# Kernel tuning notes

Measured on AMD Instinct MI355X. Metric: run time of the kernel, lower is better.

Reference implementation:

```python
import jax, jax.numpy as jnp
import numpy as np

TEMP = 0.5   # temperature from __init__
EPS = 1e-8   # torch.nn.CosineSimilarity eps


def setup_inputs() -> dict:
    key = jax.random.key(0)
    N, D = 8192, 256
    x = jax.random.normal(key, (N, D), dtype=jnp.float32)
    # pairs: each label appears exactly twice, as required for the
    # sim[~mask].reshape(N, -1) in the original to be well-formed
    y = jnp.arange(N, dtype=jnp.int32) // 2
    return {"x": x, "y": y}


def reference(x, y):
    # cosine similarity matrix: normalize once, then one NxD @ DxN matmul
    # (equivalent to CosineSimilarity(x.unsqueeze(1), x.unsqueeze(0)) without
    #  the NxNxD intermediate)
    norm = jnp.maximum(jnp.linalg.norm(x, axis=1, keepdims=True), EPS)
    xn = x / norm
    sim = (xn @ xn.T) / TEMP                     # [N, N]

    # Original: positives = equal-label entries (row-major order, includes the
    # diagonal), logits = [positives | negatives] which is just a per-row
    # permutation of sim; labels = 0 -> CE target is the FIRST equal-label
    # column of each row. logsumexp is over the full row (all N entries).
    eq = y[:, None] == y[None, :]                # [N, N] bool
    first_pos = jnp.argmax(eq, axis=1)           # first column j with y_j == y_i
    target = jnp.take_along_axis(sim, first_pos[:, None], axis=1)[:, 0]  # [N]

    lse = jax.nn.logsumexp(sim, axis=1)          # [N]
    N = x.shape[0]
    loss = jnp.sum(lse - target) / N             # CrossEntropyLoss(sum) / N
    return loss
```

## Files before the change

kernel.cpp:

```cpp
#include <hip/hip_runtime.h>
#include <hip/hip_bf16.h>

#define D 256
#define INV_TEMP 2.0f

typedef __attribute__((ext_vector_type(8))) short short8;
typedef __attribute__((ext_vector_type(4))) float floatx4;

__device__ __forceinline__ unsigned short f2bf(float f) {
    union { float f; unsigned u; } a; a.f = f;
    unsigned r = (a.u + 0x7fffu + ((a.u >> 16) & 1u)) >> 16;
    return (unsigned short)r;
}

__device__ __forceinline__ void gload_lds16(const unsigned short* g,
                                            unsigned short* l) {
    __builtin_amdgcn_global_load_lds(
        (const __attribute__((address_space(1))) unsigned int*)g,
        (__attribute__((address_space(3))) unsigned int*)l, 16, 0, 0);
}

__global__ void nt_prep_kernel(const float* __restrict__ x,
                               unsigned short* __restrict__ xnb,
                               float* __restrict__ pair_dot) {
    int p    = blockIdx.x * 4 + (threadIdx.x >> 6);
    int lane = threadIdx.x & 63;
    const float4* a4 = (const float4*)(x + (size_t)(2 * p) * D);
    const float4* b4 = (const float4*)(x + (size_t)(2 * p + 1) * D);
    float4 a = a4[lane], b = b4[lane];
    float saa = a.x * a.x + a.y * a.y + a.z * a.z + a.w * a.w;
    float sbb = b.x * b.x + b.y * b.y + b.z * b.z + b.w * b.w;
    float sab = a.x * b.x + a.y * b.y + a.z * b.z + a.w * b.w;
    #pragma unroll
    for (int off = 32; off; off >>= 1) {
        saa += __shfl_xor(saa, off);
        sbb += __shfl_xor(sbb, off);
        sab += __shfl_xor(sab, off);
    }
    float inva = 1.0f / fmaxf(sqrtf(saa), 1e-8f);
    float invb = 1.0f / fmaxf(sqrtf(sbb), 1e-8f);
    ushort4 oa, ob;
    oa.x = f2bf(a.x * inva); oa.y = f2bf(a.y * inva);
    oa.z = f2bf(a.z * inva); oa.w = f2bf(a.w * inva);
    ob.x = f2bf(b.x * invb); ob.y = f2bf(b.y * invb);
    ob.z = f2bf(b.z * invb); ob.w = f2bf(b.w * invb);
    ((ushort4*)(xnb + (size_t)(2 * p) * D))[lane] = oa;
    ((ushort4*)(xnb + (size_t)(2 * p + 1) * D))[lane] = ob;
    if (lane == 0)
        pair_dot[p] = sab * inva * invb * INV_TEMP;
}

__global__ __launch_bounds__(256, 2)
void nt_simexp_kernel(const unsigned short* __restrict__ xnb,
                      float* __restrict__ contrib) {
    __shared__ __align__(16) unsigned short Bs[128 * 256];
    __shared__ __align__(16) unsigned short As[2][128 * 32];

    const int p  = blockIdx.x >> 4, q = blockIdx.x & 15;
    const int s1 = 63 - p;
    const int c0 = 64 - p;
    const int q0 = (p + q) & 15;

    const int tid  = threadIdx.x;
    const int wave = tid >> 6, lane = tid & 63;
    const int wm   = wave & 1, wn = wave >> 1;
    const int quad = lane >> 4, c = lane & 15;

    auto strip_of = [&](int i) { return (i < c0) ? p : s1; };
    auto bi_of    = [&](int i) { return (i < c0) ? (p + i) : (s1 + i - c0); };

    auto load_B = [&](int bj) {
        const unsigned short* src = xnb + (size_t)(bj * 128) * D;
        int rs = lane >> 5, pp = lane & 31;
        #pragma unroll
        for (int t = 0; t < 16; ++t) {
            int wl = wave * 16 + t;
            int rr = wl * 2 + rs;
            int j  = (pp & ~7) | ((pp ^ rr) & 7);
            gload_lds16(src + (size_t)rr * D + j * 8, Bs + wl * 512 + lane * 8);
        }
    };
    auto load_A = [&](int bi, int ph, unsigned short* Ab) {
        const unsigned short* src = xnb + (size_t)(bi * 128) * D + ph * 32;
        int rl = lane >> 2, pq = lane & 3;
        #pragma unroll
        for (int t = 0; t < 2; ++t) {
            int wl = wave * 2 + t;
            int rr = wl * 16 + rl;
            int j  = pq ^ ((rr >> 1) & 3);
            gload_lds16(src + (size_t)rr * D + j * 8, Ab + wl * 512 + lane * 8);
        }
    };

    floatx4 acc[4][4];
    auto compute = [&](const unsigned short* Ab, int ph) {
        const int pA = quad ^ ((c >> 1) & 3);
        const int jg = ph * 4 + quad;
        const int pB = (jg & ~7) | ((jg ^ c) & 7);
        short8 af[4], bf[4];
        #pragma unroll
        for (int mt = 0; mt < 4; ++mt)
            af[mt] = *(const short8*)(Ab + (wm * 64 + mt * 16 + c) * 32 + pA * 8);
        #pragma unroll
        for (int nt = 0; nt < 4; ++nt)
            bf[nt] = *(const short8*)(Bs + (wn * 64 + nt * 16 + c) * 256 + pB * 8);
        #pragma unroll
        for (int mt = 0; mt < 4; ++mt)
            #pragma unroll
            for (int nt = 0; nt < 4; ++nt)
                acc[mt][nt] = __builtin_amdgcn_mfma_f32_16x16x32_bf16(
                    af[mt], bf[nt], acc[mt][nt], 0, 0, 0);
    };

    int bj = strip_of(q0);
    load_B(bj);
    load_A(bi_of(q0), 0, As[0]);
    __syncthreads();

    for (int i = q0; i < 65; i += 16) {
        const int bi = bi_of(i);
        const int ni = i + 16;
        const bool have_next = (ni < 65);
        const int nbj = have_next ? strip_of(ni) : -1;
        const bool same = have_next && (nbj == bj);

        #pragma unroll
        for (int mt = 0; mt < 4; ++mt)
            #pragma unroll
            for (int nt = 0; nt < 4; ++nt)
                acc[mt][nt] = (floatx4){0.f, 0.f, 0.f, 0.f};

        #pragma unroll
        for (int ph = 0; ph < 8; ++ph) {
            if (ph < 7) load_A(bi, ph + 1, As[(ph + 1) & 1]);
            else if (same) load_A(bi_of(ni), 0, As[0]);
            compute(As[ph & 1], ph);
            __syncthreads();
        }

        if (have_next && !same) {
            load_B(nbj);
            load_A(bi_of(ni), 0, As[0]);
        }

        #pragma unroll
        for (int mt = 0; mt < 4; ++mt)
            #pragma unroll
            for (int nt = 0; nt < 4; ++nt)
                #pragma unroll
                for (int r = 0; r < 4; ++r)
                    acc[mt][nt][r] = __expf(acc[mt][nt][r] * INV_TEMP);

        #pragma unroll
        for (int mt = 0; mt < 4; ++mt) {
            float ps[4] = {0.f, 0.f, 0.f, 0.f};
            #pragma unroll
            for (int nt = 0; nt < 4; ++nt)
                #pragma unroll
                for (int r = 0; r < 4; ++r)
                    ps[r] += acc[mt][nt][r];
            #pragma unroll
            for (int off = 1; off < 16; off <<= 1)
                #pragma unroll
                for (int r = 0; r < 4; ++r)
                    ps[r] += __shfl_xor(ps[r], off);
            if (c == 0) {
                float4 v = {ps[0], ps[1], ps[2], ps[3]};
                *(float4*)(contrib + (((size_t)bi * 64 + bj) * 2 + wn) * 128 +
                           wm * 64 + mt * 16 + quad * 4) = v;
            }
        }
        if (bi != bj) {
            #pragma unroll
            for (int nt = 0; nt < 4; ++nt) {
                float cs = 0.f;
                #pragma unroll
                for (int mt = 0; mt < 4; ++mt)
                    #pragma unroll
                    for (int r = 0; r < 4; ++r)
                        cs += acc[mt][nt][r];
                cs += __shfl_xor(cs, 16);
                cs += __shfl_xor(cs, 32);
                if (quad == 0)
                    contrib[(((size_t)bj * 64 + bi) * 2 + wm) * 128 +
                            wn * 64 + nt * 16 + c] = cs;
            }
        }
        if (have_next && !same) {
            __syncthreads();
            bj = nbj;
        }
    }
}

__global__ void nt_reduce_kernel(const float* __restrict__ contrib,
                                 const float* __restrict__ pair_dot,
                                 float* __restrict__ blockPart) {
    __shared__ float sm[256];
    int b  = blockIdx.x;
    int rl = threadIdx.x & 127, h = threadIdx.x >> 7;
    float s = 0.f;
    const float* base = contrib + (((size_t)b * 64) * 2 + h) * 128 + rl;
    #pragma unroll
    for (int j = 0; j < 64; ++j) s += base[(size_t)j * 256];
    sm[threadIdx.x] = s;
    __syncthreads();
    float v = 0.f;
    if (h == 0) v = logf(sm[rl] + sm[128 + rl]);
    else if (rl < 64) v = -pair_dot[b * 64 + rl];
    __syncthreads();
    sm[threadIdx.x] = v;
    __syncthreads();
    for (int st = 128; st; st >>= 1) {
        if ((int)threadIdx.x < st) sm[threadIdx.x] += sm[threadIdx.x + st];
        __syncthreads();
    }
    if (threadIdx.x == 0) blockPart[b] = sm[0];
}

__global__ void nt_final_kernel(const float* __restrict__ blockPart,
                                float* __restrict__ out, int N) {
    int lane = threadIdx.x & 63;
    float s = blockPart[lane];
    #pragma unroll
    for (int off = 32; off; off >>= 1) s += __shfl_xor(s, off);
    if (lane == 0) out[0] = (s - (float)N) / (float)N;
}

extern "C" void kernel_launch(void* const* d_in, const int* in_sizes, int n_in,
                              void* d_out, int out_size, void* d_ws, size_t ws_size,
                              hipStream_t stream) {
    const float* x = (const float*)d_in[0];
    int N = in_sizes[0] / D;

    char* ws = (char*)d_ws;
    unsigned short* xnb = (unsigned short*)ws;
    float* pair_dot  = (float*)(ws + (size_t)N * D * 2);
    float* contrib   = pair_dot + N / 2;
    float* blockPart = contrib + (size_t)64 * 64 * 2 * 128;

    nt_prep_kernel<<<N / 8, 256, 0, stream>>>(x, xnb, pair_dot);
    nt_simexp_kernel<<<512, 256, 0, stream>>>(xnb, contrib);
    nt_reduce_kernel<<<N / 128, 256, 0, stream>>>(contrib, pair_dot, blockPart);
    nt_final_kernel<<<1, 64, 0, stream>>>(blockPart, (float*)d_out, N);
}
```

Before: 100.9 us.

## Load A fragments directly from global into registers and fuse final reduction via atomics

The GEMM kernel drops the LDS staging buffer for A and instead loads A fragments straight from global memory into double-buffered registers. B fragments are also prefetched into registers one phase ahead, which removes the per-phase __syncthreads. Separately, the reduce kernel now uses vectorized float4 loads, and the last block (found through an atomic counter) writes the final loss, removing the separate final kernel launch. The risks are exposed global-load latency on A and atomic float-summation order nondeterminism.

```diff
diff --git a/kernel.cpp b/kernel.cpp
--- a/kernel.cpp
+++ b/kernel.cpp
@@ -22,7 +22,10 @@
 
 __global__ void nt_prep_kernel(const float* __restrict__ x,
                                unsigned short* __restrict__ xnb,
-                               float* __restrict__ pair_dot) {
+                               float* __restrict__ pair_dot,
+                               float* __restrict__ gsum,
+                               unsigned int* __restrict__ gcnt) {
+    if (blockIdx.x == 0 && threadIdx.x == 0) { *gsum = 0.f; *gcnt = 0u; }
     int p    = blockIdx.x * 4 + (threadIdx.x >> 6);
     int lane = threadIdx.x & 63;
     const float4* a4 = (const float4*)(x + (size_t)(2 * p) * D);
@@ -54,7 +57,6 @@
 void nt_simexp_kernel(const unsigned short* __restrict__ xnb,
                       float* __restrict__ contrib) {
     __shared__ __align__(16) unsigned short Bs[128 * 256];
-    __shared__ __align__(16) unsigned short As[2][128 * 32];
 
     const int p  = blockIdx.x >> 4, q = blockIdx.x & 15;
     const int s1 = 63 - p;
@@ -80,42 +82,31 @@
             gload_lds16(src + (size_t)rr * D + j * 8, Bs + wl * 512 + lane * 8);
         }
     };
-    auto load_A = [&](int bi, int ph, unsigned short* Ab) {
-        const unsigned short* src = xnb + (size_t)(bi * 128) * D + ph * 32;
-        int rl = lane >> 2, pq = lane & 3;
-        #pragma unroll
-        for (int t = 0; t < 2; ++t) {
-            int wl = wave * 2 + t;
-            int rr = wl * 16 + rl;
-            int j  = pq ^ ((rr >> 1) & 3);
-            gload_lds16(src + (size_t)rr * D + j * 8, Ab + wl * 512 + lane * 8);
-        }
+
+    short8 abuf[2][4], bbuf[2][4];
+
+    auto load_a = [&](short8* dst, int bi, int ph) {
+        const unsigned short* src = xnb + (size_t)(bi * 128 + wm * 64 + c) * D
+                                        + ph * 32 + quad * 8;
+        #pragma unroll
+        for (int mt = 0; mt < 4; ++mt)
+            dst[mt] = *(const short8*)(src + mt * 16 * D);
     };
-
-    floatx4 acc[4][4];
-    auto compute = [&](const unsigned short* Ab, int ph) {
-        const int pA = quad ^ ((c >> 1) & 3);
+    auto load_b = [&](short8* dst, int ph) {
         const int jg = ph * 4 + quad;
         const int pB = (jg & ~7) | ((jg ^ c) & 7);
-        short8 af[4], bf[4];
-        #pragma unroll
-        for (int mt = 0; mt < 4; ++mt)
-            af[mt] = *(const short8*)(Ab + (wm * 64 + mt * 16 + c) * 32 + pA * 8);
         #pragma unroll
         for (int nt = 0; nt < 4; ++nt)
-            bf[nt] = *(const short8*)(Bs + (wn * 64 + nt * 16 + c) * 256 + pB * 8);
-        #pragma unroll
-        for (int mt = 0; mt < 4; ++mt)
-            #pragma unroll
-            for (int nt = 0; nt < 4; ++nt)
-                acc[mt][nt] = __builtin_amdgcn_mfma_f32_16x16x32_bf16(
-                    af[mt], bf[nt], acc[mt][nt], 0, 0, 0);
+            dst[nt] = *(const short8*)(Bs + (wn * 64 + nt * 16 + c) * D + pB * 8);
     };
+
+    floatx4 acc[4][4];
 
     int bj = strip_of(q0);
     load_B(bj);
-    load_A(bi_of(q0), 0, As[0]);
+    load_a(abuf[0], bi_of(q0), 0);
     __syncthreads();
+    load_b(bbuf[0], 0);
 
     for (int i = q0; i < 65; i += 16) {
         const int bi = bi_of(i);
@@ -132,15 +123,26 @@
 
         #pragma unroll
         for (int ph = 0; ph < 8; ++ph) {
-            if (ph < 7) load_A(bi, ph + 1, As[(ph + 1) & 1]);
-            else if (same) load_A(bi_of(ni), 0, As[0]);
-            compute(As[ph & 1], ph);
+            const int cur = ph & 1, nxt = cur ^ 1;
+            if (ph < 7) {
+                load_a(abuf[nxt], bi, ph + 1);
+                load_b(bbuf[nxt], ph + 1);
+            } else if (same) {
+                load_a(abuf[0], bi_of(ni), 0);
+                load_b(bbuf[0], 0);
+            }
+            #pragma unroll
+            for (int mt = 0; mt < 4; ++mt)
+                #pragma unroll
+                for (int nt = 0; nt < 4; ++nt)
+                    acc[mt][nt] = __builtin_amdgcn_mfma_f32_16x16x32_bf16(
+                        abuf[cur][mt], bbuf[cur][nt], acc[mt][nt], 0, 0, 0);
+        }
+
+        if (have_next && !same) {
             __syncthreads();
-        }
-
-        if (have_next && !same) {
             load_B(nbj);
-            load_A(bi_of(ni), 0, As[0]);
+            load_a(abuf[0], bi_of(ni), 0);
         }
 
         #pragma unroll
@@ -189,42 +191,60 @@
         if (have_next && !same) {
             __syncthreads();
             bj = nbj;
+            load_b(bbuf[0], 0);
         }
     }
 }
 
 __global__ void nt_reduce_kernel(const float* __restrict__ contrib,
                                  const float* __restrict__ pair_dot,
-                                 float* __restrict__ blockPart) {
+                                 float* __restrict__ gsum,
+                                 unsigned int* __restrict__ gcnt,
+                                 float* __restrict__ out, int N) {
     __shared__ float sm[256];
+    __shared__ __align__(16) float rs[2][128];
     int b  = blockIdx.x;
-    int rl = threadIdx.x & 127, h = threadIdx.x >> 7;
-    float s = 0.f;
-    const float* base = contrib + (((size_t)b * 64) * 2 + h) * 128 + rl;
+    int jp = threadIdx.x & 3;
+    int idx = threadIdx.x >> 2;
+    int h  = idx >> 5, rg = idx & 31;
+    const float* base = contrib + (((size_t)b * 64 + jp) * 2 + h) * 128 + rg * 4;
+    float4 s = {0.f, 0.f, 0.f, 0.f};
     #pragma unroll
-    for (int j = 0; j < 64; ++j) s += base[(size_t)j * 256];
-    sm[threadIdx.x] = s;
+    for (int j16 = 0; j16 < 16; ++j16) {
+        float4 v = *(const float4*)(base + (size_t)j16 * 1024);
+        s.x += v.x; s.y += v.y; s.z += v.z; s.w += v.w;
+    }
+    #pragma unroll
+    for (int off = 1; off < 4; off <<= 1) {
+        s.x += __shfl_xor(s.x, off);
+        s.y += __shfl_xor(s.y, off);
+        s.z += __shfl_xor(s.z, off);
+        s.w += __shfl_xor(s.w, off);
+    }
+    if (jp == 0) {
+        float4 v = {s.x, s.y, s.z, s.w};
+        *(float4*)&rs[h][rg * 4] = v;
+    }
     __syncthreads();
     float v = 0.f;
-    if (h == 0) v = logf(sm[rl] + sm[128 + rl]);
-    else if (rl < 64) v = -pair_dot[b * 64 + rl];
-    __syncthreads();
+    int rl = threadIdx.x & 127;
+    if (threadIdx.x < 128) v = logf(rs[0][rl] + rs[1][rl]);
+    else if (rl < 64)      v = -pair_dot[b * 64 + rl];
     sm[threadIdx.x] = v;
     __syncthreads();
     for (int st = 128; st; st >>= 1) {
         if ((int)threadIdx.x < st) sm[threadIdx.x] += sm[threadIdx.x + st];
         __syncthreads();
     }
-    if (threadIdx.x == 0) blockPart[b] = sm[0];
-}
-
-__global__ void nt_final_kernel(const float* __restrict__ blockPart,
-                                float* __restrict__ out, int N) {
-    int lane = threadIdx.x & 63;
-    float s = blockPart[lane];
-    #pragma unroll
-    for (int off = 32; off; off >>= 1) s += __shfl_xor(s, off);
-    if (lane == 0) out[0] = (s - (float)N) / (float)N;
+    if (threadIdx.x == 0) {
+        atomicAdd(gsum, sm[0]);
+        __threadfence();
+        if (atomicAdd(gcnt, 1u) == 63u) {
+            __threadfence();
+            float tot = atomicAdd(gsum, 0.0f);
+            out[0] = (tot - (float)N) / (float)N;
+        }
+    }
 }
 
 extern "C" void kernel_launch(void* const* d_in, const int* in_sizes, int n_in,
@@ -237,10 +257,11 @@
     unsigned short* xnb = (unsigned short*)ws;
     float* pair_dot  = (float*)(ws + (size_t)N * D * 2);
     float* contrib   = pair_dot + N / 2;
-    float* blockPart = contrib + (size_t)64 * 64 * 2 * 128;
-
-    nt_prep_kernel<<<N / 8, 256, 0, stream>>>(x, xnb, pair_dot);
+    float* gsum      = contrib + (size_t)64 * 64 * 2 * 128;
+    unsigned int* gcnt = (unsigned int*)(gsum + 1);
+
+    nt_prep_kernel<<<N / 8, 256, 0, stream>>>(x, xnb, pair_dot, gsum, gcnt);
     nt_simexp_kernel<<<512, 256, 0, stream>>>(xnb, contrib);
-    nt_reduce_kernel<<<N / 128, 256, 0, stream>>>(contrib, pair_dot, blockPart);
-    nt_final_kernel<<<1, 64, 0, stream>>>(blockPart, (float*)d_out, N);
-}
+    nt_reduce_kernel<<<N / 128, 256, 0, stream>>>(contrib, pair_dot, gsum, gcnt,
+                                                  (float*)d_out, N);
+}
```

Measured after the change: 113.8 us. 1.13x slower.

## Accumulate row sums with atomics and fold final reduction into reduce kernel

Applied to the files above, without the earlier changes.

The GEMM+exp kernel now adds each tile's partial row and column sums directly into an N-length rowsum buffer with atomics. This replaces writing a large per-tile contrib array that a separate pass had to read back. The reduce kernel becomes a small 16-block kernel that takes log of each row sum, subtracts the pair dot products, and finishes the scalar through a global atomic sum and a last-block counter, so the separate final kernel is gone. Zeroing of the accumulators moves into the prep kernel. The prep kernel's normalized bf16 stores also become nontemporal, which risks evicting data from cache just before the GEMM reads it back; the atomics add contention and make the summation order nondeterministic.

```diff
diff --git a/kernel.cpp b/kernel.cpp
--- a/kernel.cpp
+++ b/kernel.cpp
@@ -6,6 +6,7 @@
 
 typedef __attribute__((ext_vector_type(8))) short short8;
 typedef __attribute__((ext_vector_type(4))) float floatx4;
+typedef __attribute__((ext_vector_type(4))) unsigned short ushortx4;
 
 __device__ __forceinline__ unsigned short f2bf(float f) {
     union { float f; unsigned u; } a; a.f = f;
@@ -22,7 +23,12 @@
 
 __global__ void nt_prep_kernel(const float* __restrict__ x,
                                unsigned short* __restrict__ xnb,
-                               float* __restrict__ pair_dot) {
+                               float* __restrict__ pair_dot,
+                               float* __restrict__ rowsum,
+                               float* __restrict__ gsum,
+                               unsigned int* __restrict__ gcnt) {
+    if (blockIdx.x == 0 && threadIdx.x == 0) { *gsum = 0.f; *gcnt = 0u; }
+    if (blockIdx.x < 32) rowsum[blockIdx.x * 256 + threadIdx.x] = 0.f;
     int p    = blockIdx.x * 4 + (threadIdx.x >> 6);
     int lane = threadIdx.x & 63;
     const float4* a4 = (const float4*)(x + (size_t)(2 * p) * D);
@@ -39,20 +45,20 @@
     }
     float inva = 1.0f / fmaxf(sqrtf(saa), 1e-8f);
     float invb = 1.0f / fmaxf(sqrtf(sbb), 1e-8f);
-    ushort4 oa, ob;
+    ushortx4 oa, ob;
     oa.x = f2bf(a.x * inva); oa.y = f2bf(a.y * inva);
     oa.z = f2bf(a.z * inva); oa.w = f2bf(a.w * inva);
     ob.x = f2bf(b.x * invb); ob.y = f2bf(b.y * invb);
     ob.z = f2bf(b.z * invb); ob.w = f2bf(b.w * invb);
-    ((ushort4*)(xnb + (size_t)(2 * p) * D))[lane] = oa;
-    ((ushort4*)(xnb + (size_t)(2 * p + 1) * D))[lane] = ob;
+    __builtin_nontemporal_store(oa, (ushortx4*)(xnb + (size_t)(2 * p) * D) + lane);
+    __builtin_nontemporal_store(ob, (ushortx4*)(xnb + (size_t)(2 * p + 1) * D) + lane);
     if (lane == 0)
         pair_dot[p] = sab * inva * invb * INV_TEMP;
 }
 
 __global__ __launch_bounds__(256, 2)
 void nt_simexp_kernel(const unsigned short* __restrict__ xnb,
-                      float* __restrict__ contrib) {
+                      float* __restrict__ rowsum) {
     __shared__ __align__(16) unsigned short Bs[128 * 256];
     __shared__ __align__(16) unsigned short As[2][128 * 32];
 
@@ -164,10 +170,10 @@
                 #pragma unroll
                 for (int r = 0; r < 4; ++r)
                     ps[r] += __shfl_xor(ps[r], off);
-            if (c == 0) {
-                float4 v = {ps[0], ps[1], ps[2], ps[3]};
-                *(float4*)(contrib + (((size_t)bi * 64 + bj) * 2 + wn) * 128 +
-                           wm * 64 + mt * 16 + quad * 4) = v;
+            if (c < 4) {
+                float v = (c == 0) ? ps[0] : (c == 1) ? ps[1]
+                        : (c == 2) ? ps[2] : ps[3];
+                atomicAdd(&rowsum[bi * 128 + wm * 64 + mt * 16 + quad * 4 + c], v);
             }
         }
         if (bi != bj) {
@@ -182,8 +188,7 @@
                 cs += __shfl_xor(cs, 16);
                 cs += __shfl_xor(cs, 32);
                 if (quad == 0)
-                    contrib[(((size_t)bj * 64 + bi) * 2 + wm) * 128 +
-                            wn * 64 + nt * 16 + c] = cs;
+                    atomicAdd(&rowsum[bj * 128 + wn * 64 + nt * 16 + c], cs);
             }
         }
         if (have_next && !same) {
@@ -193,38 +198,31 @@
     }
 }
 
-__global__ void nt_reduce_kernel(const float* __restrict__ contrib,
+__global__ void nt_reduce_kernel(const float* __restrict__ rowsum,
                                  const float* __restrict__ pair_dot,
-                                 float* __restrict__ blockPart) {
-    __shared__ float sm[256];
-    int b  = blockIdx.x;
-    int rl = threadIdx.x & 127, h = threadIdx.x >> 7;
-    float s = 0.f;
-    const float* base = contrib + (((size_t)b * 64) * 2 + h) * 128 + rl;
+                                 float* __restrict__ gsum,
+                                 unsigned int* __restrict__ gcnt,
+                                 float* __restrict__ out, int N) {
+    __shared__ float sm[8];
+    int r = blockIdx.x * 512 + threadIdx.x;
+    float v = logf(rowsum[r]);
+    if (r & 1) v -= pair_dot[r >> 1];
     #pragma unroll
-    for (int j = 0; j < 64; ++j) s += base[(size_t)j * 256];
-    sm[threadIdx.x] = s;
+    for (int off = 32; off; off >>= 1) v += __shfl_xor(v, off);
+    int lane = threadIdx.x & 63, wv = threadIdx.x >> 6;
+    if (lane == 0) sm[wv] = v;
     __syncthreads();
-    float v = 0.f;
-    if (h == 0) v = logf(sm[rl] + sm[128 + rl]);
-    else if (rl < 64) v = -pair_dot[b * 64 + rl];
-    __syncthreads();
-    sm[threadIdx.x] = v;
-    __syncthreads();
-    for (int st = 128; st; st >>= 1) {
-        if ((int)threadIdx.x < st) sm[threadIdx.x] += sm[threadIdx.x + st];
-        __syncthreads();
+    if (threadIdx.x == 0) {
+        float s = sm[0] + sm[1] + sm[2] + sm[3]
+                + sm[4] + sm[5] + sm[6] + sm[7];
+        atomicAdd(gsum, s);
+        __threadfence();
+        if (atomicAdd(gcnt, 1u) == 15u) {
+            __threadfence();
+            float t = atomicAdd(gsum, 0.0f);
+            out[0] = (t - (float)N) / (float)N;
+        }
     }
-    if (threadIdx.x == 0) blockPart[b] = sm[0];
-}
-
-__global__ void nt_final_kernel(const float* __restrict__ blockPart,
-                                float* __restrict__ out, int N) {
-    int lane = threadIdx.x & 63;
-    float s = blockPart[lane];
-    #pragma unroll
-    for (int off = 32; off; off >>= 1) s += __shfl_xor(s, off);
-    if (lane == 0) out[0] = (s - (float)N) / (float)N;
 }
 
 extern "C" void kernel_launch(void* const* d_in, const int* in_sizes, int n_in,
@@ -236,11 +234,13 @@
     char* ws = (char*)d_ws;
     unsigned short* xnb = (unsigned short*)ws;
     float* pair_dot  = (float*)(ws + (size_t)N * D * 2);
-    float* contrib   = pair_dot + N / 2;
-    float* blockPart = contrib + (size_t)64 * 64 * 2 * 128;
-
-    nt_prep_kernel<<<N / 8, 256, 0, stream>>>(x, xnb, pair_dot);
-    nt_simexp_kernel<<<512, 256, 0, stream>>>(xnb, contrib);
-    nt_reduce_kernel<<<N / 128, 256, 0, stream>>>(contrib, pair_dot, blockPart);
-    nt_final_kernel<<<1, 64, 0, stream>>>(blockPart, (float*)d_out, N);
-}
+    float* rowsum    = pair_dot + N / 2;
+    float* gsum      = rowsum + N;
+    unsigned int* gcnt = (unsigned int*)(gsum + 1);
+
+    nt_prep_kernel<<<N / 8, 256, 0, stream>>>(x, xnb, pair_dot, rowsum,
+                                              gsum, gcnt);
+    nt_simexp_kernel<<<512, 256, 0, stream>>>(xnb, rowsum);
+    nt_reduce_kernel<<<16, 512, 0, stream>>>(rowsum, pair_dot, gsum, gcnt,
+                                             (float*)d_out, N);
+}
```

Result: no change. 101.8 us (+0.9%).
